# Performance work log

Hardware: AMD Instinct MI355X
Metric: run time of the kernel (lower is better)

The kernel has to match this reference:

```python
import jax, jax.numpy as jnp
import numpy as np


def _gru_layer(x, w_ih, w_hh, b_ih, b_hh):
    """PyTorch-semantics GRU over x:[B,T,I]. w_ih:[3H,I], w_hh:[3H,H]."""
    B, T, I = x.shape
    H = w_hh.shape[1]
    # precompute input-side gates for all timesteps: [T,B,3H]
    gx = (jnp.einsum('bti,gi->btg', x, w_ih) + b_ih).transpose(1, 0, 2)

    def step(h, gx_t):
        gh = h @ w_hh.T + b_hh  # [B,3H]
        xr, xz, xn = jnp.split(gx_t, 3, axis=-1)
        hr, hz, hn = jnp.split(gh, 3, axis=-1)
        r = jax.nn.sigmoid(xr + hr)
        z = jax.nn.sigmoid(xz + hz)
        n = jnp.tanh(xn + r * hn)
        h_new = (1.0 - z) * n + z * h
        return h_new, h_new

    h0 = jnp.zeros((B, H), dtype=x.dtype)
    _, hs = jax.lax.scan(step, h0, gx)  # hs: [T,B,H]
    return hs.transpose(1, 0, 2)


def _gru_params(key, in_size, hidden):
    k = 1.0 / np.sqrt(hidden)
    k1, k2, k3, k4 = jax.random.split(key, 4)
    w_ih = jax.random.uniform(k1, (3 * hidden, in_size), minval=-k, maxval=k, dtype=jnp.float32)
    w_hh = jax.random.uniform(k2, (3 * hidden, hidden), minval=-k, maxval=k, dtype=jnp.float32)
    b_ih = jax.random.uniform(k3, (3 * hidden,), minval=-k, maxval=k, dtype=jnp.float32)
    b_hh = jax.random.uniform(k4, (3 * hidden,), minval=-k, maxval=k, dtype=jnp.float32)
    return w_ih, w_hh, b_ih, b_hh


def setup_inputs() -> dict:
    key = jax.random.key(0)
    ks = jax.random.split(key, 6)
    B, T = 256, 1024
    x = jax.random.normal(ks[0], (B, T), dtype=jnp.float32)
    sizes = [(1, 256), (256, 128), (128, 128), (128, 256)]
    d = {'x': x}
    for i, (isz, h) in enumerate(sizes):
        w_ih, w_hh, b_ih, b_hh = _gru_params(ks[1 + i], isz, h)
        d[f'w_ih{i+1}'] = w_ih
        d[f'w_hh{i+1}'] = w_hh
        d[f'b_ih{i+1}'] = b_ih
        d[f'b_hh{i+1}'] = b_hh
    kw, kb = jax.random.split(ks[5])
    kk = 1.0 / np.sqrt(256.0)
    d['w_out'] = jax.random.uniform(kw, (1, 256), minval=-kk, maxval=kk, dtype=jnp.float32)
    d['b_out'] = jax.random.uniform(kb, (1,), minval=-kk, maxval=kk, dtype=jnp.float32)
    return d


def reference(x, w_ih1, w_hh1, b_ih1, b_hh1,
              w_ih2, w_hh2, b_ih2, b_hh2,
              w_ih3, w_hh3, b_ih3, b_hh3,
              w_ih4, w_hh4, b_ih4, b_hh4,
              w_out, b_out):
    h = x[..., None]  # [B,T,1]
    h = _gru_layer(h, w_ih1, w_hh1, b_ih1, b_hh1)
    h = _gru_layer(h, w_ih2, w_hh2, b_ih2, b_hh2)
    h = _gru_layer(h, w_ih3, w_hh3, b_ih3, b_hh3)
    h = _gru_layer(h, w_ih4, w_hh4, b_ih4, b_hh4)
    y = jnp.einsum('bth,oh->bto', h, w_out) + b_out  # TimeDistributed Linear(256,1)
    return y.reshape(y.shape[0], -1)  # flatten from dim 1 -> [B,T]
```

## Files before the change

kernel.cpp:

```cpp
#include <hip/hip_runtime.h>
#include <math.h>


__device__ __forceinline__ float sigmoidf_(float v) {
    return 1.0f / (1.0f + __expf(-v));
}

__global__ void prep_k(const float* __restrict__ src, float* __restrict__ dst,
                       int H, int J) {
    int idx = blockIdx.x * 256 + threadIdx.x;
    int total = 3 * H * J;
    if (idx < total) {
        int g = idx / (H * J);
        int rem = idx - g * H * J;
        int u = rem / J;
        int j = rem - u * J;
        dst[(u * 3 + g) * J + j] = src[(g * H + u) * J + j];
    }
}


__device__ __forceinline__ void flag_st(int* p, int v) {
    __hip_atomic_store(p, v, __ATOMIC_RELAXED, __HIP_MEMORY_SCOPE_AGENT);
}
__device__ __forceinline__ int flag_ld(const int* p) {
    return __hip_atomic_load(p, __ATOMIC_RELAXED, __HIP_MEMORY_SCOPE_AGENT);
}
__device__ __forceinline__ void ex_store(float* p, float v) {
    __hip_atomic_store(p, v, __ATOMIC_RELAXED, __HIP_MEMORY_SCOPE_AGENT);
}

__device__ __forceinline__ void pollwait(const int* p, int tgt, bool active) {
    if (threadIdx.x < 64) {
        int spins = 0;
        while (true) {
            int v = active ? flag_ld(p) : 0x7fffffff;
            if (__all(v >= tgt)) break;
            if (++spins > 200000) break;
            __builtin_amdgcn_s_sleep(1);
        }
    }
    __syncthreads();
}

template <int J>
__device__ __forceinline__ void stageX(float* dst, const float* src) {
    constexpr int NF4 = (32 * J) / 1024;
    constexpr int LJ = (J == 256) ? 8 : 7;
    float4 tmp[NF4];
    #pragma unroll
    for (int k = 0; k < NF4; ++k) {
        const float* p = src + (size_t)(k * 256 + threadIdx.x) * 4;
        asm volatile("global_load_dwordx4 %0, %1, off sc0 sc1"
                     : "=v"(tmp[k]) : "v"(p) : "memory");
    }
    asm volatile("s_waitcnt vmcnt(0)" ::: "memory");
    #pragma unroll
    for (int k = 0; k < NF4; ++k) {
        int i = (k * 256 + threadIdx.x) * 4;
        int b = i >> LJ;
        int j = i & (J - 1);
        *(float4*)(dst + b * (J + 4) + j) = tmp[k];
    }
}

template <int J>
__device__ __forceinline__ void zero32(float* dst) {
    for (int i = threadIdx.x; i < 32 * (J + 4); i += 256) dst[i] = 0.0f;
}

template <int KB, int J>
__device__ __forceinline__ void dot3(const float* __restrict__ w3,
                                     const float* __restrict__ hst, int b0,
                                     float* ar, float* az, float* ac) {
    const float4* wr = (const float4*)w3;
    const float4* wz = (const float4*)(w3 + J);
    const float4* wn = (const float4*)(w3 + 2 * J);
    const float* rows[KB];
    #pragma unroll
    for (int k = 0; k < KB; ++k) rows[k] = hst + (b0 + k * (32 / KB)) * (J + 4);
    #pragma unroll 4
    for (int j4 = 0; j4 < J / 4; ++j4) {
        float4 a = wr[j4];
        float4 c = wz[j4];
        float4 d = wn[j4];
        #pragma unroll
        for (int k = 0; k < KB; ++k) {
            float4 hv = *(const float4*)(rows[k] + j4 * 4);
            ar[k] = fmaf(hv.x, a.x, ar[k]); ar[k] = fmaf(hv.y, a.y, ar[k]);
            ar[k] = fmaf(hv.z, a.z, ar[k]); ar[k] = fmaf(hv.w, a.w, ar[k]);
            az[k] = fmaf(hv.x, c.x, az[k]); az[k] = fmaf(hv.y, c.y, az[k]);
            az[k] = fmaf(hv.z, c.z, az[k]); az[k] = fmaf(hv.w, c.w, az[k]);
            ac[k] = fmaf(hv.x, d.x, ac[k]); ac[k] = fmaf(hv.y, d.y, ac[k]);
            ac[k] = fmaf(hv.z, d.z, ac[k]); ac[k] = fmaf(hv.w, d.w, ac[k]);
        }
    }
}

__global__ __launch_bounds__(256) void gru_pipe_kernel(
    const float* __restrict__ x,
    const float* __restrict__ w_ih1,
    const float* __restrict__ b_ih1, const float* __restrict__ b_hh1,
    const float* __restrict__ b_ih2, const float* __restrict__ b_hh2,
    const float* __restrict__ b_ih3, const float* __restrict__ b_hh3,
    const float* __restrict__ b_ih4, const float* __restrict__ b_hh4,
    const float* __restrict__ wA_hh1,
    const float* __restrict__ wA_ih2,
    const float* __restrict__ wA_hh2,
    const float* __restrict__ wA_ih3,
    const float* __restrict__ wA_hh3,
    const float* __restrict__ wA_ih4,
    const float* __restrict__ wA_hh4,
    const float* __restrict__ w_out, const float* __restrict__ b_out,
    int* __restrict__ flags,
    float* __restrict__ ex,
    float* __restrict__ out)
{
    const int tid = threadIdx.x;
    extern __shared__ float smem[];
    __shared__ float xs[32];
    __shared__ float wsum[4][4][8];

    const int bg = blockIdx.x & 7;
    const int rest = blockIdx.x >> 3;
    const int s = rest >> 3;
    const int us = rest & 7;

    int* fb = flags + bg * 128;
    int* arr_own = fb + s * 32;

    const int* pT = arr_own; int dT = -1000000000; bool aT = false;
    const int* pM = arr_own; int dM = -1000000000; bool aM = false;
    if (tid < 8) {
        if (s > 0) { pT = fb + (s - 1) * 32 + tid; dT = 1; aT = true; }
        pM = arr_own + tid; dM = 0; aM = true;
    } else if (tid < 16) {
        if (s < 3) { pT = fb + (s + 1) * 32 + (tid - 8); dT = -3; aT = true; }
    }

    float* exb = ex + (size_t)bg * 98304;
    float* h1r = exb;
    float* h2r = exb + 32768;
    float* h3r = exb + 49152;
    float* h4r = exb + 65536;

    if (s == 0) {
        float* wlds = smem;
        float* hprev = smem + 24704;
        {
            const float* srcw = wA_hh1 + (size_t)us * 32 * 768;
            for (int i = tid; i < 24576; i += 256) {
                int uu = i / 768, r = i - uu * 768;
                wlds[uu * 772 + r] = srcw[i];
            }
        }
        __syncthreads();
        const int ul = tid >> 3, b0 = tid & 7;
        const int u = us * 32 + ul;
        const float* wh = wlds + ul * 772;
        const float br = b_ih1[u] + b_hh1[u];
        const float bz = b_ih1[u + 256] + b_hh1[u + 256];
        const float bxn = b_ih1[u + 512];
        const float bhn = b_hh1[u + 512];
        const float wir = w_ih1[u], wiz = w_ih1[u + 256], win = w_ih1[u + 512];
        for (int t = 0; t < 1024; ++t) {
            pollwait(pT, t + dT, aT);
            if (tid < 32) xs[tid] = x[(size_t)(bg * 32 + tid) * 1024 + t];
            pollwait(pM, t + dM, aM);
            if (t > 0) stageX<256>(hprev, h1r + (size_t)((t - 1) & 3) * 8192);
            else       zero32<256>(hprev);
            __syncthreads();
            float ar[4], az[4], axn[4], ahn[4];
            #pragma unroll
            for (int k = 0; k < 4; ++k) {
                float xv = xs[b0 + 8 * k];
                ar[k] = br + xv * wir; az[k] = bz + xv * wiz;
                axn[k] = bxn + xv * win; ahn[k] = bhn;
            }
            dot3<4, 256>(wh, hprev, b0, ar, az, ahn);
            float* hout = h1r + (size_t)(t & 3) * 8192;
            #pragma unroll
            for (int k = 0; k < 4; ++k) {
                int b = b0 + 8 * k;
                float hp = hprev[b * 260 + u];
                float r = sigmoidf_(ar[k]);
                float z = sigmoidf_(az[k]);
                float n = tanhf(axn[k] + r * ahn[k]);
                ex_store(hout + b * 256 + u, (1.f - z) * n + z * hp);
            }
            asm volatile("s_waitcnt vmcnt(0)" ::: "memory");
            __syncthreads();
            if (tid == 0) flag_st(arr_own + us, t + 1);
        }
    } else if (s == 1) {
        float* wlds = smem;
        float* hin = smem + 6208;
        float* hprev = smem + 14528;
        {
            const float* srcw = wA_hh2 + (size_t)us * 16 * 384;
            for (int i = tid; i < 6144; i += 256) {
                int uu = i / 384, r = i - uu * 384;
                wlds[uu * 388 + r] = srcw[i];
            }
        }
        __syncthreads();
        const int ul = tid >> 4, b0 = tid & 15;
        const int u = us * 16 + ul;
        const float* wi = wA_ih2 + (size_t)u * 768;
        const float* wh = wlds + ul * 388;
        const float br = b_ih2[u] + b_hh2[u];
        const float bz = b_ih2[u + 128] + b_hh2[u + 128];
        const float bxn = b_ih2[u + 256];
        const float bhn = b_hh2[u + 256];
        for (int t = 0; t < 1024; ++t) {
            pollwait(pT, t + dT, aT);
            stageX<256>(hin, h1r + (size_t)(t & 3) * 8192);
            __syncthreads();
            float ar[2] = {br, br}, az[2] = {bz, bz};
            float axn[2] = {bxn, bxn}, ahn[2] = {bhn, bhn};
            dot3<2, 256>(wi, hin, b0, ar, az, axn);
            pollwait(pM, t + dM, aM);
            if (t > 0) stageX<128>(hprev, h2r + (size_t)((t - 1) & 3) * 4096);
            else       zero32<128>(hprev);
            __syncthreads();
            dot3<2, 128>(wh, hprev, b0, ar, az, ahn);
            float* hout = h2r + (size_t)(t & 3) * 4096;
            #pragma unroll
            for (int k = 0; k < 2; ++k) {
                int b = b0 + 16 * k;
                float hp = hprev[b * 132 + u];
                float r = sigmoidf_(ar[k]);
                float z = sigmoidf_(az[k]);
                float n = tanhf(axn[k] + r * ahn[k]);
                ex_store(hout + b * 128 + u, (1.f - z) * n + z * hp);
            }
            asm volatile("s_waitcnt vmcnt(0)" ::: "memory");
            __syncthreads();
            if (tid == 0) flag_st(arr_own + us, t + 1);
        }
    } else if (s == 2) {
        float* wlds = smem;
        float* hin = smem + 6208;
        float* hprev = smem + 10432;
        {
            const float* srcw = wA_hh3 + (size_t)us * 16 * 384;
            for (int i = tid; i < 6144; i += 256) {
                int uu = i / 384, r = i - uu * 384;
                wlds[uu * 388 + r] = srcw[i];
            }
        }
        __syncthreads();
        const int ul = tid >> 4, b0 = tid & 15;
        const int u = us * 16 + ul;
        const float* wi = wA_ih3 + (size_t)u * 384;
        const float* wh = wlds + ul * 388;
        const float br = b_ih3[u] + b_hh3[u];
        const float bz = b_ih3[u + 128] + b_hh3[u + 128];
        const float bxn = b_ih3[u + 256];
        const float bhn = b_hh3[u + 256];
        for (int t = 0; t < 1024; ++t) {
            pollwait(pT, t + dT, aT);
            stageX<128>(hin, h2r + (size_t)(t & 3) * 4096);
            __syncthreads();
            float ar[2] = {br, br}, az[2] = {bz, bz};
            float axn[2] = {bxn, bxn}, ahn[2] = {bhn, bhn};
            dot3<2, 128>(wi, hin, b0, ar, az, axn);
            pollwait(pM, t + dM, aM);
            if (t > 0) stageX<128>(hprev, h3r + (size_t)((t - 1) & 3) * 4096);
            else       zero32<128>(hprev);
            __syncthreads();
            dot3<2, 128>(wh, hprev, b0, ar, az, ahn);
            float* hout = h3r + (size_t)(t & 3) * 4096;
            #pragma unroll
            for (int k = 0; k < 2; ++k) {
                int b = b0 + 16 * k;
                float hp = hprev[b * 132 + u];
                float r = sigmoidf_(ar[k]);
                float z = sigmoidf_(az[k]);
                float n = tanhf(axn[k] + r * ahn[k]);
                ex_store(hout + b * 128 + u, (1.f - z) * n + z * hp);
            }
            asm volatile("s_waitcnt vmcnt(0)" ::: "memory");
            __syncthreads();
            if (tid == 0) flag_st(arr_own + us, t + 1);
        }
    } else {
        float* wlds = smem;
        float* hin = smem + 24704;
        float* hprev = smem + 28928;
        {
            const float* srcw = wA_hh4 + (size_t)us * 32 * 768;
            for (int i = tid; i < 24576; i += 256) {
                int uu = i / 768, r = i - uu * 768;
                wlds[uu * 772 + r] = srcw[i];
            }
        }
        __syncthreads();
        const int ul = tid >> 3, b0 = tid & 7;
        const int u = us * 32 + ul;
        const float* wi = wA_ih4 + (size_t)u * 384;
        const float* wh = wlds + ul * 772;
        const float br = b_ih4[u] + b_hh4[u];
        const float bz = b_ih4[u + 256] + b_hh4[u + 256];
        const float bxn = b_ih4[u + 512];
        const float bhn = b_hh4[u + 512];
        const float wo = w_out[u];
        for (int t = 0; t < 1024; ++t) {
            pollwait(pT, t + dT, aT);
            stageX<128>(hin, h3r + (size_t)(t & 3) * 4096);
            __syncthreads();
            float ar[4], az[4], axn[4], ahn[4];
            #pragma unroll
            for (int k = 0; k < 4; ++k) {
                ar[k] = br; az[k] = bz; axn[k] = bxn; ahn[k] = bhn;
            }
            dot3<4, 128>(wi, hin, b0, ar, az, axn);
            pollwait(pM, t + dM, aM);
            if (t > 0) stageX<256>(hprev, h4r + (size_t)((t - 1) & 3) * 8192);
            else       zero32<256>(hprev);
            __syncthreads();
            dot3<4, 256>(wh, hprev, b0, ar, az, ahn);
            float* hout = h4r + (size_t)(t & 3) * 8192;
            float pk[4];
            #pragma unroll
            for (int k = 0; k < 4; ++k) {
                int b = b0 + 8 * k;
                float hp = hprev[b * 260 + u];
                float r = sigmoidf_(ar[k]);
                float z = sigmoidf_(az[k]);
                float n = tanhf(axn[k] + r * ahn[k]);
                float hnew = (1.f - z) * n + z * hp;
                ex_store(hout + b * 256 + u, hnew);
                pk[k] = wo * hnew;
            }
            #pragma unroll
            for (int k = 0; k < 4; ++k) {
                pk[k] += __shfl_xor(pk[k], 8, 64);
                pk[k] += __shfl_xor(pk[k], 16, 64);
                pk[k] += __shfl_xor(pk[k], 32, 64);
            }
            if ((tid & 63) < 8) {
                int w = tid >> 6;
                #pragma unroll
                for (int k = 0; k < 4; ++k) wsum[w][k][tid & 7] = pk[k];
            }
            asm volatile("s_waitcnt vmcnt(0)" ::: "memory");
            __syncthreads();
            if (tid == 0) flag_st(arr_own + us, t + 1);
            if (tid < 32) {
                int k = tid >> 3, bb = tid & 7;
                float ssum = wsum[0][k][bb] + wsum[1][k][bb] +
                             wsum[2][k][bb] + wsum[3][k][bb];
                if (us == 0) ssum += b_out[0];
                atomicAdd(out + (size_t)(bg * 32 + bb + 8 * k) * 1024 + t, ssum);
            }
        }
    }
}

extern "C" void kernel_launch(void* const* d_in, const int* in_sizes, int n_in,
                              void* d_out, int out_size, void* d_ws, size_t ws_size,
                              hipStream_t stream) {
    const float* x     = (const float*)d_in[0];
    const float* w_ih1 = (const float*)d_in[1];
    const float* w_hh1 = (const float*)d_in[2];
    const float* b_ih1 = (const float*)d_in[3];
    const float* b_hh1 = (const float*)d_in[4];
    const float* w_ih2 = (const float*)d_in[5];
    const float* w_hh2 = (const float*)d_in[6];
    const float* b_ih2 = (const float*)d_in[7];
    const float* b_hh2 = (const float*)d_in[8];
    const float* w_ih3 = (const float*)d_in[9];
    const float* w_hh3 = (const float*)d_in[10];
    const float* b_ih3 = (const float*)d_in[11];
    const float* b_hh3 = (const float*)d_in[12];
    const float* w_ih4 = (const float*)d_in[13];
    const float* w_hh4 = (const float*)d_in[14];
    const float* b_ih4 = (const float*)d_in[15];
    const float* b_hh4 = (const float*)d_in[16];
    const float* w_out = (const float*)d_in[17];
    const float* b_out = (const float*)d_in[18];

    float* ws = (float*)d_ws;
    float* wA_hh1 = ws;
    float* wA_ih2 = wA_hh1 + 196608;
    float* wA_hh2 = wA_ih2 + 98304;
    float* wA_ih3 = wA_hh2 + 49152;
    float* wA_hh3 = wA_ih3 + 49152;
    float* wA_ih4 = wA_hh3 + 49152;
    float* wA_hh4 = wA_ih4 + 98304;
    float* ex     = wA_hh4 + 196608;
    int*   flags  = (int*)(ex + 786432);

    hipMemsetAsync(flags, 0, 1024 * sizeof(int), stream);
    hipMemsetAsync(d_out, 0, 256 * 1024 * sizeof(float), stream);

    prep_k<<<768, 256, 0, stream>>>(w_hh1, wA_hh1, 256, 256);
    prep_k<<<384, 256, 0, stream>>>(w_ih2, wA_ih2, 128, 256);
    prep_k<<<192, 256, 0, stream>>>(w_hh2, wA_hh2, 128, 128);
    prep_k<<<192, 256, 0, stream>>>(w_ih3, wA_ih3, 128, 128);
    prep_k<<<192, 256, 0, stream>>>(w_hh3, wA_hh3, 128, 128);
    prep_k<<<384, 256, 0, stream>>>(w_ih4, wA_ih4, 256, 128);
    prep_k<<<768, 256, 0, stream>>>(w_hh4, wA_hh4, 256, 256);

    const int dyn_lds = 37248 * (int)sizeof(float);
    (void)hipFuncSetAttribute((const void*)gru_pipe_kernel,
                              hipFuncAttributeMaxDynamicSharedMemorySize, dyn_lds);

    gru_pipe_kernel<<<256, 256, dyn_lds, stream>>>(
        x, w_ih1, b_ih1, b_hh1, b_ih2, b_hh2, b_ih3, b_hh3, b_ih4, b_hh4,
        wA_hh1, wA_ih2, wA_hh2, wA_ih3, wA_hh3, wA_ih4, wA_hh4,
        w_out, b_out, flags, ex, (float*)d_out);
}
```

Baseline: 18.21 ms.

## Merge per-step waits, stage both inputs together, vectorize hidden-state exchange stores

Each pipeline stage now does one combined poll for its upstream, downstream and own-layer flags instead of two separate waits. It then loads the next-layer input and its own previous hidden state in a single batch of global loads before the dot products. The exchange buffer layout changes to unit-major with contiguous batch entries, so each thread writes its 2 or 4 outputs with one dwordx2/x4 store instead of several scalar atomic stores. Layers 2 and 3 also keep their input weights in LDS. The intent is fewer synchronization round-trips and memory transactions on the serial per-timestep critical path. The cost is a transposing scatter into LDS and a combined wait that holds the stage until every dependency is ready.

```diff
diff --git a/kernel.cpp b/kernel.cpp
--- a/kernel.cpp
+++ b/kernel.cpp
@@ -1,6 +1,9 @@
 #include <hip/hip_runtime.h>
 #include <math.h>
 
+
+typedef float vf4 __attribute__((ext_vector_type(4)));
+typedef float vf2 __attribute__((ext_vector_type(2)));
 
 __device__ __forceinline__ float sigmoidf_(float v) {
     return 1.0f / (1.0f + __expf(-v));
@@ -26,9 +29,6 @@
 __device__ __forceinline__ int flag_ld(const int* p) {
     return __hip_atomic_load(p, __ATOMIC_RELAXED, __HIP_MEMORY_SCOPE_AGENT);
 }
-__device__ __forceinline__ void ex_store(float* p, float v) {
-    __hip_atomic_store(p, v, __ATOMIC_RELAXED, __HIP_MEMORY_SCOPE_AGENT);
-}
 
 __device__ __forceinline__ void pollwait(const int* p, int tgt, bool active) {
     if (threadIdx.x < 64) {
@@ -44,24 +44,46 @@
 }
 
 template <int J>
-__device__ __forceinline__ void stageX(float* dst, const float* src) {
-    constexpr int NF4 = (32 * J) / 1024;
-    constexpr int LJ = (J == 256) ? 8 : 7;
-    float4 tmp[NF4];
+__device__ __forceinline__ void ld_chunks(vf4* t, const float* src) {
+    constexpr int N = (32 * J) / 1024;
     #pragma unroll
-    for (int k = 0; k < NF4; ++k) {
+    for (int k = 0; k < N; ++k) {
         const float* p = src + (size_t)(k * 256 + threadIdx.x) * 4;
         asm volatile("global_load_dwordx4 %0, %1, off sc0 sc1"
-                     : "=v"(tmp[k]) : "v"(p) : "memory");
-    }
+                     : "=v"(t[k]) : "v"(p) : "memory");
+    }
+}
+template <int J>
+__device__ __forceinline__ void wr_chunks(float* dst, const vf4* t) {
+    constexpr int N = (32 * J) / 1024;
+    #pragma unroll
+    for (int k = 0; k < N; ++k) {
+        int i = (k * 256 + threadIdx.x) * 4;
+        int u = i >> 5;
+        int b4 = i & 31;
+        dst[(b4 + 0) * (J + 4) + u] = t[k].x;
+        dst[(b4 + 1) * (J + 4) + u] = t[k].y;
+        dst[(b4 + 2) * (J + 4) + u] = t[k].z;
+        dst[(b4 + 3) * (J + 4) + u] = t[k].w;
+    }
+}
+template <int J1, int J2>
+__device__ __forceinline__ void stagePair(float* d1, const float* s1,
+                                          float* d2, const float* s2) {
+    vf4 t1[(32 * J1) / 1024];
+    vf4 t2[(32 * J2) / 1024];
+    ld_chunks<J1>(t1, s1);
+    ld_chunks<J2>(t2, s2);
     asm volatile("s_waitcnt vmcnt(0)" ::: "memory");
-    #pragma unroll
-    for (int k = 0; k < NF4; ++k) {
-        int i = (k * 256 + threadIdx.x) * 4;
-        int b = i >> LJ;
-        int j = i & (J - 1);
-        *(float4*)(dst + b * (J + 4) + j) = tmp[k];
-    }
+    wr_chunks<J1>(d1, t1);
+    wr_chunks<J2>(d2, t2);
+}
+template <int J>
+__device__ __forceinline__ void stageOne(float* d, const float* s) {
+    vf4 t[(32 * J) / 1024];
+    ld_chunks<J>(t, s);
+    asm volatile("s_waitcnt vmcnt(0)" ::: "memory");
+    wr_chunks<J>(d, t);
 }
 
 template <int J>
@@ -71,14 +93,14 @@
 
 template <int KB, int J>
 __device__ __forceinline__ void dot3(const float* __restrict__ w3,
-                                     const float* __restrict__ hst, int b0,
+                                     const float* __restrict__ hst, int b00,
                                      float* ar, float* az, float* ac) {
     const float4* wr = (const float4*)w3;
     const float4* wz = (const float4*)(w3 + J);
     const float4* wn = (const float4*)(w3 + 2 * J);
     const float* rows[KB];
     #pragma unroll
-    for (int k = 0; k < KB; ++k) rows[k] = hst + (b0 + k * (32 / KB)) * (J + 4);
+    for (int k = 0; k < KB; ++k) rows[k] = hst + (b00 + k) * (J + 4);
     #pragma unroll 4
     for (int j4 = 0; j4 < J / 4; ++j4) {
         float4 a = wr[j4];
@@ -95,6 +117,15 @@
             ac[k] = fmaf(hv.z, d.z, ac[k]); ac[k] = fmaf(hv.w, d.w, ac[k]);
         }
     }
+}
+
+__device__ __forceinline__ void st_x4(float* p, vf4 v) {
+    asm volatile("global_store_dwordx4 %0, %1, off sc0 sc1"
+                 :: "v"(p), "v"(v) : "memory");
+}
+__device__ __forceinline__ void st_x2(float* p, vf2 v) {
+    asm volatile("global_store_dwordx2 %0, %1, off sc0 sc1"
+                 :: "v"(p), "v"(v) : "memory");
 }
 
 __global__ __launch_bounds__(256) void gru_pipe_kernel(
@@ -129,13 +160,13 @@
     int* fb = flags + bg * 128;
     int* arr_own = fb + s * 32;
 
-    const int* pT = arr_own; int dT = -1000000000; bool aT = false;
-    const int* pM = arr_own; int dM = -1000000000; bool aM = false;
+    const int* pp = arr_own; int dd = -1000000000; bool act = false;
     if (tid < 8) {
-        if (s > 0) { pT = fb + (s - 1) * 32 + tid; dT = 1; aT = true; }
-        pM = arr_own + tid; dM = 0; aM = true;
+        if (s > 0) { pp = fb + (s - 1) * 32 + tid; dd = 1; act = true; }
     } else if (tid < 16) {
-        if (s < 3) { pT = fb + (s + 1) * 32 + (tid - 8); dT = -3; aT = true; }
+        if (s < 3) { pp = fb + (s + 1) * 32 + (tid - 8); dd = -3; act = true; }
+    } else if (tid < 24) {
+        pp = fb + s * 32 + (tid - 16); dd = 0; act = true;
     }
 
     float* exb = ex + (size_t)bg * 98304;
@@ -156,6 +187,7 @@
         }
         __syncthreads();
         const int ul = tid >> 3, b0 = tid & 7;
+        const int b00 = b0 * 4;
         const int u = us * 32 + ul;
         const float* wh = wlds + ul * 772;
         const float br = b_ih1[u] + b_hh1[u];
@@ -164,122 +196,139 @@
         const float bhn = b_hh1[u + 512];
         const float wir = w_ih1[u], wiz = w_ih1[u + 256], win = w_ih1[u + 512];
         for (int t = 0; t < 1024; ++t) {
-            pollwait(pT, t + dT, aT);
+            pollwait(pp, t + dd, act);
             if (tid < 32) xs[tid] = x[(size_t)(bg * 32 + tid) * 1024 + t];
-            pollwait(pM, t + dM, aM);
-            if (t > 0) stageX<256>(hprev, h1r + (size_t)((t - 1) & 3) * 8192);
+            if (t > 0) stageOne<256>(hprev, h1r + (size_t)((t - 1) & 3) * 8192);
             else       zero32<256>(hprev);
             __syncthreads();
             float ar[4], az[4], axn[4], ahn[4];
             #pragma unroll
             for (int k = 0; k < 4; ++k) {
-                float xv = xs[b0 + 8 * k];
+                float xv = xs[b00 + k];
                 ar[k] = br + xv * wir; az[k] = bz + xv * wiz;
                 axn[k] = bxn + xv * win; ahn[k] = bhn;
             }
-            dot3<4, 256>(wh, hprev, b0, ar, az, ahn);
-            float* hout = h1r + (size_t)(t & 3) * 8192;
+            dot3<4, 256>(wh, hprev, b00, ar, az, ahn);
+            vf4 ho;
             #pragma unroll
             for (int k = 0; k < 4; ++k) {
-                int b = b0 + 8 * k;
-                float hp = hprev[b * 260 + u];
+                float hp = hprev[(b00 + k) * 260 + u];
                 float r = sigmoidf_(ar[k]);
                 float z = sigmoidf_(az[k]);
                 float n = tanhf(axn[k] + r * ahn[k]);
-                ex_store(hout + b * 256 + u, (1.f - z) * n + z * hp);
-            }
+                ho[k] = (1.f - z) * n + z * hp;
+            }
+            st_x4(h1r + (size_t)(t & 3) * 8192 + (size_t)u * 32 + b00, ho);
             asm volatile("s_waitcnt vmcnt(0)" ::: "memory");
             __syncthreads();
             if (tid == 0) flag_st(arr_own + us, t + 1);
         }
     } else if (s == 1) {
-        float* wlds = smem;
-        float* hin = smem + 6208;
-        float* hprev = smem + 14528;
+        float* whh = smem;
+        float* wih = smem + 6208;
+        float* hin = smem + 18560;
+        float* hprev = smem + 26880;
         {
             const float* srcw = wA_hh2 + (size_t)us * 16 * 384;
             for (int i = tid; i < 6144; i += 256) {
                 int uu = i / 384, r = i - uu * 384;
-                wlds[uu * 388 + r] = srcw[i];
+                whh[uu * 388 + r] = srcw[i];
+            }
+            const float* srci = wA_ih2 + (size_t)us * 16 * 768;
+            for (int i = tid; i < 12288; i += 256) {
+                int uu = i / 768, r = i - uu * 768;
+                wih[uu * 772 + r] = srci[i];
             }
         }
         __syncthreads();
         const int ul = tid >> 4, b0 = tid & 15;
+        const int b00 = b0 * 2;
         const int u = us * 16 + ul;
-        const float* wi = wA_ih2 + (size_t)u * 768;
-        const float* wh = wlds + ul * 388;
+        const float* wi = wih + ul * 772;
+        const float* wh = whh + ul * 388;
         const float br = b_ih2[u] + b_hh2[u];
         const float bz = b_ih2[u + 128] + b_hh2[u + 128];
         const float bxn = b_ih2[u + 256];
         const float bhn = b_hh2[u + 256];
         for (int t = 0; t < 1024; ++t) {
-            pollwait(pT, t + dT, aT);
-            stageX<256>(hin, h1r + (size_t)(t & 3) * 8192);
+            pollwait(pp, t + dd, act);
+            if (t > 0) {
+                stagePair<256, 128>(hin, h1r + (size_t)(t & 3) * 8192,
+                                    hprev, h2r + (size_t)((t - 1) & 3) * 4096);
+            } else {
+                stageOne<256>(hin, h1r);
+                zero32<128>(hprev);
+            }
             __syncthreads();
             float ar[2] = {br, br}, az[2] = {bz, bz};
             float axn[2] = {bxn, bxn}, ahn[2] = {bhn, bhn};
-            dot3<2, 256>(wi, hin, b0, ar, az, axn);
-            pollwait(pM, t + dM, aM);
-            if (t > 0) stageX<128>(hprev, h2r + (size_t)((t - 1) & 3) * 4096);
-            else       zero32<128>(hprev);
-            __syncthreads();
-            dot3<2, 128>(wh, hprev, b0, ar, az, ahn);
-            float* hout = h2r + (size_t)(t & 3) * 4096;
+            dot3<2, 256>(wi, hin, b00, ar, az, axn);
+            dot3<2, 128>(wh, hprev, b00, ar, az, ahn);
+            vf2 ho;
             #pragma unroll
             for (int k = 0; k < 2; ++k) {
-                int b = b0 + 16 * k;
-                float hp = hprev[b * 132 + u];
+                float hp = hprev[(b00 + k) * 132 + u];
                 float r = sigmoidf_(ar[k]);
                 float z = sigmoidf_(az[k]);
                 float n = tanhf(axn[k] + r * ahn[k]);
-                ex_store(hout + b * 128 + u, (1.f - z) * n + z * hp);
-            }
+                ho[k] = (1.f - z) * n + z * hp;
+            }
+            st_x2(h2r + (size_t)(t & 3) * 4096 + (size_t)u * 32 + b00, ho);
             asm volatile("s_waitcnt vmcnt(0)" ::: "memory");
             __syncthreads();
             if (tid == 0) flag_st(arr_own + us, t + 1);
         }
     } else if (s == 2) {
-        float* wlds = smem;
-        float* hin = smem + 6208;
-        float* hprev = smem + 10432;
+        float* whh = smem;
+        float* wih = smem + 6208;
+        float* hin = smem + 12416;
+        float* hprev = smem + 16640;
         {
             const float* srcw = wA_hh3 + (size_t)us * 16 * 384;
             for (int i = tid; i < 6144; i += 256) {
                 int uu = i / 384, r = i - uu * 384;
-                wlds[uu * 388 + r] = srcw[i];
+                whh[uu * 388 + r] = srcw[i];
+            }
+            const float* srci = wA_ih3 + (size_t)us * 16 * 384;
+            for (int i = tid; i < 6144; i += 256) {
+                int uu = i / 384, r = i - uu * 384;
+                wih[uu * 388 + r] = srci[i];
             }
         }
         __syncthreads();
         const int ul = tid >> 4, b0 = tid & 15;
+        const int b00 = b0 * 2;
         const int u = us * 16 + ul;
-        const float* wi = wA_ih3 + (size_t)u * 384;
-        const float* wh = wlds + ul * 388;
+        const float* wi = wih + ul * 388;
+        const float* wh = whh + ul * 388;
         const float br = b_ih3[u] + b_hh3[u];
         const float bz = b_ih3[u + 128] + b_hh3[u + 128];
         const float bxn = b_ih3[u + 256];
         const float bhn = b_hh3[u + 256];
         for (int t = 0; t < 1024; ++t) {
-            pollwait(pT, t + dT, aT);
-            stageX<128>(hin, h2r + (size_t)(t & 3) * 4096);
+            pollwait(pp, t + dd, act);
+            if (t > 0) {
+                stagePair<128, 128>(hin, h2r + (size_t)(t & 3) * 4096,
+                                    hprev, h3r + (size_t)((t - 1) & 3) * 4096);
+            } else {
+                stageOne<128>(hin, h2r);
+                zero32<128>(hprev);
+            }
             __syncthreads();
             float ar[2] = {br, br}, az[2] = {bz, bz};
             float axn[2] = {bxn, bxn}, ahn[2] = {bhn, bhn};
-            dot3<2, 128>(wi, hin, b0, ar, az, axn);
-            pollwait(pM, t + dM, aM);
-            if (t > 0) stageX<128>(hprev, h3r + (size_t)((t - 1) & 3) * 4096);
-            else       zero32<128>(hprev);
-            __syncthreads();
-            dot3<2, 128>(wh, hprev, b0, ar, az, ahn);
-            float* hout = h3r + (size_t)(t & 3) * 4096;
+            dot3<2, 128>(wi, hin, b00, ar, az, axn);
+            dot3<2, 128>(wh, hprev, b00, ar, az, ahn);
+            vf2 ho;
             #pragma unroll
             for (int k = 0; k < 2; ++k) {
-                int b = b0 + 16 * k;
-                float hp = hprev[b * 132 + u];
+                float hp = hprev[(b00 + k) * 132 + u];
                 float r = sigmoidf_(ar[k]);
                 float z = sigmoidf_(az[k]);
                 float n = tanhf(axn[k] + r * ahn[k]);
-                ex_store(hout + b * 128 + u, (1.f - z) * n + z * hp);
-            }
+                ho[k] = (1.f - z) * n + z * hp;
+            }
+            st_x2(h3r + (size_t)(t & 3) * 4096 + (size_t)u * 32 + b00, ho);
             asm volatile("s_waitcnt vmcnt(0)" ::: "memory");
             __syncthreads();
             if (tid == 0) flag_st(arr_own + us, t + 1);
@@ -297,6 +346,7 @@
         }
         __syncthreads();
         const int ul = tid >> 3, b0 = tid & 7;
+        const int b00 = b0 * 4;
         const int u = us * 32 + ul;
         const float* wi = wA_ih4 + (size_t)u * 384;
         const float* wh = wlds + ul * 772;
@@ -306,33 +356,35 @@
         const float bhn = b_hh4[u + 512];
         const float wo = w_out[u];
         for (int t = 0; t < 1024; ++t) {
-            pollwait(pT, t + dT, aT);
-            stageX<128>(hin, h3r + (size_t)(t & 3) * 4096);
+            pollwait(pp, t + dd, act);
+            if (t > 0) {
+                stagePair<128, 256>(hin, h3r + (size_t)(t & 3) * 4096,
+                                    hprev, h4r + (size_t)((t - 1) & 3) * 8192);
+            } else {
+                stageOne<128>(hin, h3r);
+                zero32<256>(hprev);
+            }
             __syncthreads();
             float ar[4], az[4], axn[4], ahn[4];
             #pragma unroll
             for (int k = 0; k < 4; ++k) {
                 ar[k] = br; az[k] = bz; axn[k] = bxn; ahn[k] = bhn;
             }
-            dot3<4, 128>(wi, hin, b0, ar, az, axn);
-            pollwait(pM, t + dM, aM);
-            if (t > 0) stageX<256>(hprev, h4r + (size_t)((t - 1) & 3) * 8192);
-            else       zero32<256>(hprev);
-            __syncthreads();
-            dot3<4, 256>(wh, hprev, b0, ar, az, ahn);
-            float* hout = h4r + (size_t)(t & 3) * 8192;
+            dot3<4, 128>(wi, hin, b00, ar, az, axn);
+            dot3<4, 256>(wh, hprev, b00, ar, az, ahn);
+            vf4 ho;
             float pk[4];
             #pragma unroll
             for (int k = 0; k < 4; ++k) {
-                int b = b0 + 8 * k;
-                float hp = hprev[b * 260 + u];
+                float hp = hprev[(b00 + k) * 260 + u];
                 float r = sigmoidf_(ar[k]);
                 float z = sigmoidf_(az[k]);
                 float n = tanhf(axn[k] + r * ahn[k]);
                 float hnew = (1.f - z) * n + z * hp;
-                ex_store(hout + b * 256 + u, hnew);
+                ho[k] = hnew;
                 pk[k] = wo * hnew;
             }
+            st_x4(h4r + (size_t)(t & 3) * 8192 + (size_t)u * 32 + b00, ho);
             #pragma unroll
             for (int k = 0; k < 4; ++k) {
                 pk[k] += __shfl_xor(pk[k], 8, 64);
@@ -352,7 +404,7 @@
                 float ssum = wsum[0][k][bb] + wsum[1][k][bb] +
                              wsum[2][k][bb] + wsum[3][k][bb];
                 if (us == 0) ssum += b_out[0];
-                atomicAdd(out + (size_t)(bg * 32 + bb + 8 * k) * 1024 + t, ssum);
+                atomicAdd(out + (size_t)(bg * 32 + bb * 4 + k) * 1024 + t, ssum);
             }
         }
     }
@@ -392,8 +444,8 @@
     float* ex     = wA_hh4 + 196608;
     int*   flags  = (int*)(ex + 786432);
 
-    hipMemsetAsync(flags, 0, 1024 * sizeof(int), stream);
-    hipMemsetAsync(d_out, 0, 256 * 1024 * sizeof(float), stream);
+    (void)hipMemsetAsync(flags, 0, 1024 * sizeof(int), stream);
+    (void)hipMemsetAsync(d_out, 0, 256 * 1024 * sizeof(float), stream);
 
     prep_k<<<768, 256, 0, stream>>>(w_hh1, wA_hh1, 256, 256);
     prep_k<<<384, 256, 0, stream>>>(w_ih2, wA_ih2, 128, 256);
```

After: 19.42 ms. 1.07x slower.
